# Kernel tuning notes

Measured on AMD Instinct MI355X. Metric: run time of the kernel, lower is better.

## Reference

```python
import jax, jax.numpy as jnp
import numpy as np

B, N, F = 16, 1024, 256
HEADS, K, DOUT = 8, 512, 256
TAU = 1.0
EPS = 1e-08


def setup_inputs() -> dict:
    key = jax.random.key(0)
    k1, k2, k3, k4, k5, k6 = jax.random.split(key, 6)
    return {
        'Q': jax.random.normal(k1, (B, N, F), dtype=jnp.float32),
        'keys': jax.random.uniform(k2, (HEADS, K, F), dtype=jnp.float32),
        'conv_w': jax.random.normal(k3, (HEADS,), dtype=jnp.float32),
        'lin_w': jax.random.normal(k4, (DOUT, F), dtype=jnp.float32) * 0.05,
        'lin_b': jax.random.normal(k5, (DOUT,), dtype=jnp.float32) * 0.05,
        'mask': jax.random.randint(k6, (B, N), 0, 2, dtype=jnp.int32),
    }


def kl_reg(C):
    # C: (B, N, K)
    P = C ** 2
    cn = jnp.sum(C, axis=-2, keepdims=True) + EPS          # sum over N
    P = P / cn
    pn = jnp.sum(P, axis=-1, keepdims=True) + EPS          # sum over K
    P = P / pn
    kl = jnp.sum(P * (jnp.log(P + EPS) - jnp.log(C + EPS)))
    return 100.0 * kl


def memconv_fwd(Q, keys, conv_w, lin_w, lin_b, fmask):
    # pairwise L2 distance Q (B,N,F) vs keys (H,K,F) -> C (B,H,N,K)
    q2 = jnp.sum(Q * Q, axis=-1)                            # (B,N)
    k2 = jnp.sum(keys * keys, axis=-1)                      # (H,K)
    qk = jnp.einsum('bnf,hkf->bhnk', Q, keys)               # (B,H,N,K)
    d2 = q2[:, None, :, None] + k2[None, :, None, :] - 2.0 * qk
    C = jnp.sqrt(jnp.maximum(d2, 0.0))
    em = fmask[:, None, :, None]                            # (B,1,N,1) broadcast
    C = C * em
    # student-t kernel (gmn variant)
    C = (1.0 + C ** 2 / TAU) ** (-(0.5 * TAU + 0.5))
    C = C / jnp.sum(C, axis=-1, keepdims=True)
    C = C * em
    # conv1x1 over heads -> (B,N,K)
    C = jnp.einsum('bhnk,h->bnk', C, conv_w)
    C = jax.nn.softmax(C, axis=-1)
    C = C * fmask[:, :, None]
    kl = kl_reg(C)
    V = jnp.einsum('bnk,bnf->bkf', C, Q)                    # (B,K,F)
    out = jax.nn.leaky_relu(jnp.einsum('bkf,of->bko', V, lin_w) + lin_b, 0.01)
    return out, kl


def reference(Q, keys, conv_w, lin_w, lin_b, mask):
    fmask = mask.astype(Q.dtype)
    return memconv_fwd(Q, keys, conv_w, lin_w, lin_b, fmask)
```

## Files before the change

kernel.cpp:

```cpp
#include <hip/hip_runtime.h>
#include <math.h>

#define Bc 16
#define Nc 1024
#define Fc 256
#define Hc 8
#define Kc 512
#define DOUTc 256
#define EPSc 1e-8f

typedef short v8s __attribute__((ext_vector_type(8)));
typedef float v4f __attribute__((ext_vector_type(4)));

__device__ __forceinline__ float waveReduceSum(float v) {
    v += __shfl_xor(v, 32); v += __shfl_xor(v, 16); v += __shfl_xor(v, 8);
    v += __shfl_xor(v, 4);  v += __shfl_xor(v, 2);  v += __shfl_xor(v, 1);
    return v;
}

__device__ __forceinline__ unsigned short f2bf(float f) {
    unsigned int u = __float_as_uint(f);
    u = (u + 0x7fffu + ((u >> 16) & 1u)) >> 16;
    return (unsigned short)u;
}

__device__ __forceinline__ void lds_barrier() {
    __builtin_amdgcn_s_waitcnt(0xC07F);
    __builtin_amdgcn_s_barrier();
}

__global__ __launch_bounds__(256) void prep_all(
    const float* __restrict__ Q, const float* __restrict__ keys,
    const float* __restrict__ lin_w,
    float* __restrict__ k2g, unsigned short* __restrict__ Kp,
    unsigned short* __restrict__ Qbp, unsigned short* __restrict__ Wp,
    float* __restrict__ cn, float* __restrict__ klout) {
    __shared__ unsigned short T2[32][66];
    const int bx = blockIdx.x;
    const int tid = threadIdx.x;
    if (bx < 1024) {
        int row = bx * 4 + (tid >> 6);
        int l = tid & 63;
        float4 v = *(const float4*)(keys + (size_t)row * Fc + l * 4);
        float s = v.x * v.x + v.y * v.y + v.z * v.z + v.w * v.w;
        s = waveReduceSum(s);
        if (l == 0) k2g[row] = s;
    } else if (bx < 1536) {
        int t = (bx - 1024) * 256 + tid;
        int lane = t & 63, ci = t >> 6;
        int ct = ci & 7, ks = (ci >> 3) & 7, wv = (ci >> 6) & 3, h = ci >> 8;
        int qd = lane >> 4, li = lane & 15;
        int col = h * 512 + wv * 128 + ct * 16 + li;
        const float* src = keys + (size_t)col * Fc + ks * 32 + qd * 8;
        float4 a = *(const float4*)src;
        float4 b = *(const float4*)(src + 4);
        *(ushort4*)(Kp + (size_t)t * 8) = make_ushort4(f2bf(a.x), f2bf(a.y), f2bf(a.z), f2bf(a.w));
        *(ushort4*)(Kp + (size_t)t * 8 + 4) = make_ushort4(f2bf(b.x), f2bf(b.y), f2bf(b.z), f2bf(b.w));
    } else if (bx < 3584) {
        int i = bx - 1536;
        int n0 = (i & 31) * 32, f0 = ((i >> 5) & 3) * 64, bb = i >> 7;
        {
            int n_l = tid >> 3, f_l = (tid & 7) * 8;
            const float* src = Q + ((size_t)(bb * Nc + n0 + n_l)) * Fc + f0 + f_l;
            float4 a = *(const float4*)src;
            float4 b = *(const float4*)(src + 4);
            T2[n_l][f_l + 0] = f2bf(a.x); T2[n_l][f_l + 1] = f2bf(a.y);
            T2[n_l][f_l + 2] = f2bf(a.z); T2[n_l][f_l + 3] = f2bf(a.w);
            T2[n_l][f_l + 4] = f2bf(b.x); T2[n_l][f_l + 5] = f2bf(b.y);
            T2[n_l][f_l + 6] = f2bf(b.z); T2[n_l][f_l + 7] = f2bf(b.w);
        }
        __syncthreads();
        int c = tid >> 6, L = tid & 63;
        int qd = L >> 4, li = L & 15;
        unsigned short o[8];
#pragma unroll
        for (int j = 0; j < 8; j++) o[j] = T2[qd * 8 + j][c * 16 + li];
        size_t idx = ((((size_t)bb * 16 + (f0 >> 4) + c) * 32 + (n0 >> 5)) * 64 + L) * 8;
        *(ushort4*)(Qbp + idx) = make_ushort4(o[0], o[1], o[2], o[3]);
        *(ushort4*)(Qbp + idx + 4) = make_ushort4(o[4], o[5], o[6], o[7]);
    } else if (bx < 3616) {
        int t = (bx - 3584) * 256 + tid;
        int lane = t & 63, ci = t >> 6;
        int ot = ci >> 3, fs = ci & 7;
        int qd = lane >> 4, li = lane & 15;
        const float* src = lin_w + (size_t)(ot * 16 + li) * Fc + fs * 32 + qd * 8;
        float4 a = *(const float4*)src;
        float4 b = *(const float4*)(src + 4);
        *(ushort4*)(Wp + (size_t)t * 8) = make_ushort4(f2bf(a.x), f2bf(a.y), f2bf(a.z), f2bf(a.w));
        *(ushort4*)(Wp + (size_t)t * 8 + 4) = make_ushort4(f2bf(b.x), f2bf(b.y), f2bf(b.z), f2bf(b.w));
    } else {
        int i = (bx - 3616) * 256 + tid;
        float4 z = make_float4(0.f, 0.f, 0.f, 0.f);
        float4* d = (float4*)(cn + (size_t)i * 16);
        d[0] = z; d[1] = z; d[2] = z; d[3] = z;
        if (bx == 3616 && tid == 0) *klout = 0.f;
    }
}

__global__ __launch_bounds__(256, 1) void cmfma_kernel(
    const float* __restrict__ Q, const unsigned short* __restrict__ Kp,
    const float* __restrict__ k2g, const float* __restrict__ conv_w,
    const int* __restrict__ mask, float* __restrict__ C,
    float* __restrict__ cn, unsigned short* __restrict__ Ctp) {
    __shared__ float k2s[Hc * Kc];
    __shared__ float q2s[32];
    __shared__ float msh[32];
    __shared__ float redb[Hc][4][32];
    __shared__ float mslot[4][32];
    __shared__ float eslot[4][32];
    __shared__ short Tb[512][36];
    const int tid = threadIdx.x;
    const int wv = tid >> 6, L = tid & 63;
    const int qd = L >> 4, li = L & 15;
    const int gr0 = blockIdx.x * 32;
    const int b = gr0 >> 10;

    v8s A[2][8];
    {
        float q2part[2] = {0.f, 0.f};
#pragma unroll
        for (int s = 0; s < 2; s++) {
            const float* qrow = Q + (size_t)(gr0 + s * 16 + li) * Fc + qd * 8;
#pragma unroll
            for (int ks = 0; ks < 8; ks++) {
                float4 a = *(const float4*)(qrow + ks * 32);
                float4 bq = *(const float4*)(qrow + ks * 32 + 4);
                v8s f;
                f[0] = (short)f2bf(a.x);  f[1] = (short)f2bf(a.y);
                f[2] = (short)f2bf(a.z);  f[3] = (short)f2bf(a.w);
                f[4] = (short)f2bf(bq.x); f[5] = (short)f2bf(bq.y);
                f[6] = (short)f2bf(bq.z); f[7] = (short)f2bf(bq.w);
                A[s][ks] = f;
                q2part[s] += a.x * a.x + a.y * a.y + a.z * a.z + a.w * a.w +
                             bq.x * bq.x + bq.y * bq.y + bq.z * bq.z + bq.w * bq.w;
            }
            q2part[s] += __shfl_xor(q2part[s], 16);
            q2part[s] += __shfl_xor(q2part[s], 32);
            if (qd == 0 && wv == 0) q2s[s * 16 + li] = q2part[s];
        }
    }
    if (tid < 32) msh[tid] = (float)mask[gr0 + tid];
    for (int i = tid; i < Hc * Kc / 4; i += 256)
        *(float4*)&k2s[i * 4] = *(const float4*)(k2g + i * 4);

    v4f D[2][8], S[2][8];
#pragma unroll
    for (int s = 0; s < 2; s++)
#pragma unroll
        for (int ct = 0; ct < 8; ct++) {
            D[s][ct] = (v4f){0.f, 0.f, 0.f, 0.f};
            S[s][ct] = (v4f){0.f, 0.f, 0.f, 0.f};
        }

    const unsigned short* kwbase = Kp + (size_t)L * 8;
    v8s Bc0[8], Bn[8];
    {
        const unsigned short* p0 = kwbase + (size_t)(wv * 64) * 512;
#pragma unroll
        for (int ct = 0; ct < 8; ct++) Bc0[ct] = *(const v8s*)(p0 + ct * 512);
    }

    lds_barrier();

    float q2r[2][4], mrow[2][4];
#pragma unroll
    for (int s = 0; s < 2; s++)
#pragma unroll
        for (int r = 0; r < 4; r++) {
            q2r[s][r] = q2s[s * 16 + qd * 4 + r];
            mrow[s][r] = msh[s * 16 + qd * 4 + r];
        }

#define KSTEP(kk, CUR, NXT)                                                        \
    do {                                                                           \
        int hn = h * 8 + (kk) + 1;                                                 \
        int hh = (hn >> 3) & 7, kn = hn & 7;                                       \
        const unsigned short* pb =                                                 \
            kwbase + (size_t)(((hh * 4 + wv) * 64 + kn * 8)) * 512;                \
        _Pragma("unroll") for (int ct = 0; ct < 8; ct++)                           \
            NXT[ct] = *(const v8s*)(pb + ct * 512);                                \
        _Pragma("unroll") for (int ct = 0; ct < 8; ct++)                           \
            D[0][ct] = __builtin_amdgcn_mfma_f32_16x16x32_bf16(A[0][kk], CUR[ct],  \
                                                               D[0][ct], 0, 0, 0);\
        _Pragma("unroll") for (int ct = 0; ct < 8; ct++)                           \
            D[1][ct] = __builtin_amdgcn_mfma_f32_16x16x32_bf16(A[1][kk], CUR[ct],  \
                                                               D[1][ct], 0, 0, 0);\
    } while (0)

    for (int h = 0; h < Hc; ++h) {
        KSTEP(0, Bc0, Bn); KSTEP(1, Bn, Bc0);
        KSTEP(2, Bc0, Bn); KSTEP(3, Bn, Bc0);
        KSTEP(4, Bc0, Bn); KSTEP(5, Bn, Bc0);
        KSTEP(6, Bc0, Bn); KSTEP(7, Bn, Bc0);

        float rs[2][4] = {{0.f, 0.f, 0.f, 0.f}, {0.f, 0.f, 0.f, 0.f}};
#pragma unroll
        for (int ct = 0; ct < 8; ct++) {
            float k2v = k2s[h * Kc + wv * 128 + ct * 16 + li];
#pragma unroll
            for (int s = 0; s < 2; s++)
#pragma unroll
                for (int r = 0; r < 4; r++) {
                    float d2 = fmaxf(q2r[s][r] + k2v - 2.f * D[s][ct][r], 0.f) * mrow[s][r];
                    float t = __builtin_amdgcn_rcpf(1.f + d2);
                    D[s][ct][r] = t;
                    rs[s][r] += t;
                }
        }
#pragma unroll
        for (int s = 0; s < 2; s++)
#pragma unroll
            for (int r = 0; r < 4; r++) {
                rs[s][r] += __shfl_xor(rs[s][r], 1, 16);
                rs[s][r] += __shfl_xor(rs[s][r], 2, 16);
                rs[s][r] += __shfl_xor(rs[s][r], 4, 16);
                rs[s][r] += __shfl_xor(rs[s][r], 8, 16);
            }
        if (li == 0) {
#pragma unroll
            for (int s = 0; s < 2; s++)
#pragma unroll
                for (int r = 0; r < 4; r++) redb[h][wv][s * 16 + qd * 4 + r] = rs[s][r];
        }
        lds_barrier();
        float wh = conv_w[h];
        float sc[2][4];
#pragma unroll
        for (int s = 0; s < 2; s++)
#pragma unroll
            for (int r = 0; r < 4; r++) {
                int rw = s * 16 + qd * 4 + r;
                float tot = redb[h][0][rw] + redb[h][1][rw] + redb[h][2][rw] + redb[h][3][rw];
                sc[s][r] = wh * __builtin_amdgcn_rcpf(tot);
            }
#pragma unroll
        for (int s = 0; s < 2; s++)
#pragma unroll
            for (int ct = 0; ct < 8; ct++)
#pragma unroll
                for (int r = 0; r < 4; r++) {
                    S[s][ct][r] += sc[s][r] * D[s][ct][r];
                    D[s][ct][r] = 0.f;
                }
    }
#undef KSTEP

    float mx[2][4] = {{-1e30f, -1e30f, -1e30f, -1e30f}, {-1e30f, -1e30f, -1e30f, -1e30f}};
#pragma unroll
    for (int s = 0; s < 2; s++)
#pragma unroll
        for (int ct = 0; ct < 8; ct++)
#pragma unroll
            for (int r = 0; r < 4; r++) mx[s][r] = fmaxf(mx[s][r], S[s][ct][r]);
#pragma unroll
    for (int s = 0; s < 2; s++)
#pragma unroll
        for (int r = 0; r < 4; r++) {
            mx[s][r] = fmaxf(mx[s][r], __shfl_xor(mx[s][r], 1, 16));
            mx[s][r] = fmaxf(mx[s][r], __shfl_xor(mx[s][r], 2, 16));
            mx[s][r] = fmaxf(mx[s][r], __shfl_xor(mx[s][r], 4, 16));
            mx[s][r] = fmaxf(mx[s][r], __shfl_xor(mx[s][r], 8, 16));
        }
    if (li == 0) {
#pragma unroll
        for (int s = 0; s < 2; s++)
#pragma unroll
            for (int r = 0; r < 4; r++) mslot[wv][s * 16 + qd * 4 + r] = mx[s][r];
    }
    lds_barrier();
#pragma unroll
    for (int s = 0; s < 2; s++)
#pragma unroll
        for (int r = 0; r < 4; r++) {
            int rw = s * 16 + qd * 4 + r;
            mx[s][r] = fmaxf(fmaxf(mslot[0][rw], mslot[1][rw]),
                             fmaxf(mslot[2][rw], mslot[3][rw]));
        }
    float es[2][4] = {{0.f, 0.f, 0.f, 0.f}, {0.f, 0.f, 0.f, 0.f}};
#pragma unroll
    for (int s = 0; s < 2; s++)
#pragma unroll
        for (int ct = 0; ct < 8; ct++)
#pragma unroll
            for (int r = 0; r < 4; r++) {
                float e = __expf(S[s][ct][r] - mx[s][r]);
                S[s][ct][r] = e;
                es[s][r] += e;
            }
#pragma unroll
    for (int s = 0; s < 2; s++)
#pragma unroll
        for (int r = 0; r < 4; r++) {
            es[s][r] += __shfl_xor(es[s][r], 1, 16);
            es[s][r] += __shfl_xor(es[s][r], 2, 16);
            es[s][r] += __shfl_xor(es[s][r], 4, 16);
            es[s][r] += __shfl_xor(es[s][r], 8, 16);
        }
    if (li == 0) {
#pragma unroll
        for (int s = 0; s < 2; s++)
#pragma unroll
            for (int r = 0; r < 4; r++) eslot[wv][s * 16 + qd * 4 + r] = es[s][r];
    }
    lds_barrier();
    float inv[2][4];
#pragma unroll
    for (int s = 0; s < 2; s++)
#pragma unroll
        for (int r = 0; r < 4; r++) {
            int rw = s * 16 + qd * 4 + r;
            float tot = eslot[0][rw] + eslot[1][rw] + eslot[2][rw] + eslot[3][rw];
            inv[s][r] = mrow[s][r] / tot;
        }
#pragma unroll
    for (int ct = 0; ct < 8; ct++) {
        int k = wv * 128 + ct * 16 + li;
        float colsum = 0.f;
#pragma unroll
        for (int s = 0; s < 2; s++) {
            float cv[4];
#pragma unroll
            for (int r = 0; r < 4; r++) {
                cv[r] = S[s][ct][r] * inv[s][r];
                C[(size_t)(gr0 + s * 16 + qd * 4 + r) * Kc + k] = cv[r];
                colsum += cv[r];
            }
            short4 t4;
            t4.x = (short)f2bf(cv[0]); t4.y = (short)f2bf(cv[1]);
            t4.z = (short)f2bf(cv[2]); t4.w = (short)f2bf(cv[3]);
            *(short4*)&Tb[k][s * 16 + qd * 4] = t4;
        }
        colsum += __shfl_xor(colsum, 16);
        colsum += __shfl_xor(colsum, 32);
        if (qd == 0) atomicAdd(&cn[b * Kc + k], colsum);
    }
    lds_barrier();
    {
        const int ns0 = (gr0 & 1023) >> 5;
#pragma unroll
        for (int kk = 0; kk < 2; kk++) {
            int k = tid * 2 + kk;
            int kt = k >> 4, klo = k & 15;
            size_t cbase = (((size_t)b * 32 + kt) * 32 + ns0) * 512;
#pragma unroll
            for (int q2i = 0; q2i < 4; q2i++) {
                short4 lo = *(short4*)&Tb[k][q2i * 8];
                short4 hi = *(short4*)&Tb[k][q2i * 8 + 4];
                short4* d = (short4*)(Ctp + cbase + (size_t)(q2i * 16 + klo) * 8);
                d[0] = lo; d[1] = hi;
            }
        }
    }
}

__global__ __launch_bounds__(256) void klv_kernel(
    const unsigned short* __restrict__ Ctp, const unsigned short* __restrict__ Qbp,
    unsigned short* __restrict__ Vp, const float* __restrict__ C,
    const float* __restrict__ cn, float* __restrict__ klout) {
    __shared__ short Vt[64][76];
    __shared__ float red[4];
    int tid = threadIdx.x;
    int bx = blockIdx.x;
    if (bx < 512) {
        int w = tid >> 6, L = tid & 63;
        int qd = L >> 4, li = L & 15;
        int wr = w >> 1, wc = w & 1;
        int bb = bx >> 5;
        int rem = bx & 31;
        int ktb = rem >> 2, ftb = rem & 3;
        int KT0 = ktb * 4 + wr * 2;
        int FT0 = ftb * 4 + wc * 2;
        const unsigned short* pa0 = Ctp + (((size_t)bb * 32 + KT0) * 32) * 512 + L * 8;
        const unsigned short* pa1 = pa0 + (size_t)32 * 512;
        const unsigned short* pb0 = Qbp + (((size_t)bb * 16 + FT0) * 32) * 512 + L * 8;
        const unsigned short* pb1 = pb0 + (size_t)32 * 512;
        v4f acc[2][2];
#pragma unroll
        for (int a = 0; a < 2; a++)
#pragma unroll
            for (int c = 0; c < 2; c++) acc[a][c] = (v4f){0.f, 0.f, 0.f, 0.f};

        v8s A0 = *(const v8s*)pa0, A1 = *(const v8s*)pa1;
        v8s B0 = *(const v8s*)pb0, B1 = *(const v8s*)pb1;
        for (int ns = 0; ns < 32; ns++) {
            int nsn = (ns + 1) & 31;
            v8s A0n = *(const v8s*)(pa0 + nsn * 512);
            v8s A1n = *(const v8s*)(pa1 + nsn * 512);
            v8s B0n = *(const v8s*)(pb0 + nsn * 512);
            v8s B1n = *(const v8s*)(pb1 + nsn * 512);
            acc[0][0] = __builtin_amdgcn_mfma_f32_16x16x32_bf16(A0, B0, acc[0][0], 0, 0, 0);
            acc[0][1] = __builtin_amdgcn_mfma_f32_16x16x32_bf16(A0, B1, acc[0][1], 0, 0, 0);
            acc[1][0] = __builtin_amdgcn_mfma_f32_16x16x32_bf16(A1, B0, acc[1][0], 0, 0, 0);
            acc[1][1] = __builtin_amdgcn_mfma_f32_16x16x32_bf16(A1, B1, acc[1][1], 0, 0, 0);
            A0 = A0n; A1 = A1n; B0 = B0n; B1 = B1n;
        }
#pragma unroll
        for (int a = 0; a < 2; a++)
#pragma unroll
            for (int c = 0; c < 2; c++)
#pragma unroll
                for (int r = 0; r < 4; r++)
                    Vt[(wr * 2 + a) * 16 + qd * 4 + r][(wc * 2 + c) * 16 + li] =
                        (short)f2bf(acc[a][c][r]);
        __syncthreads();
        {
            int ci = tid >> 5, s5 = tid & 31;
            int mtl = ci >> 1, fsl = ci & 1;
            size_t mt_g = (size_t)bb * 32 + ktb * 4 + mtl;
            size_t fs_g = (size_t)ftb * 2 + fsl;
#pragma unroll
            for (int half = 0; half < 2; half++) {
                int L2 = s5 + half * 32;
                int qd2 = L2 >> 4, li2 = L2 & 15;
                short4 x0 = *(short4*)&Vt[mtl * 16 + li2][fsl * 32 + qd2 * 8];
                short4 x1 = *(short4*)&Vt[mtl * 16 + li2][fsl * 32 + qd2 * 8 + 4];
                short4* d = (short4*)(Vp + ((mt_g * 8 + fs_g) * 64 + L2) * 8);
                d[0] = x0; d[1] = x1;
            }
        }
    } else {
        int bk = bx - 512;
        int w = tid >> 6, l = tid & 63;
        float kacc = 0.f;
#pragma unroll
        for (int rr = 0; rr < 4; rr++) {
            int row = bk * 16 + w * 4 + rr;
            int b = row >> 10;
            const float* cp = C + (size_t)row * Kc + l * 8;
            const float* np = cn + b * Kc + l * 8;
            float4 c0 = *(const float4*)cp;
            float4 c1 = *(const float4*)(cp + 4);
            float4 n0 = *(const float4*)np;
            float4 n1 = *(const float4*)(np + 4);
            float p[8];
            p[0] = c0.x * c0.x / (n0.x + EPSc); p[1] = c0.y * c0.y / (n0.y + EPSc);
            p[2] = c0.z * c0.z / (n0.z + EPSc); p[3] = c0.w * c0.w / (n0.w + EPSc);
            p[4] = c1.x * c1.x / (n1.x + EPSc); p[5] = c1.y * c1.y / (n1.y + EPSc);
            p[6] = c1.z * c1.z / (n1.z + EPSc); p[7] = c1.w * c1.w / (n1.w + EPSc);
            float s = p[0] + p[1] + p[2] + p[3] + p[4] + p[5] + p[6] + p[7];
            float pn = waveReduceSum(s) + EPSc;
            float rpn = 1.0f / pn;
            float cc[8] = {c0.x, c0.y, c0.z, c0.w, c1.x, c1.y, c1.z, c1.w};
#pragma unroll
            for (int j = 0; j < 8; j++) {
                float P = p[j] * rpn;
                kacc += P * __logf((P + EPSc) / (cc[j] + EPSc));
            }
        }
        kacc = waveReduceSum(kacc);
        if (l == 0) red[w] = kacc;
        __syncthreads();
        if (tid == 0)
            atomicAdd(klout, 100.f * (red[0] + red[1] + red[2] + red[3]));
    }
}

__global__ __launch_bounds__(256) void ofma_kernel(
    const unsigned short* __restrict__ Vp, const unsigned short* __restrict__ Wp,
    const float* __restrict__ bias, float* __restrict__ out) {
    int tid = threadIdx.x;
    int w = tid >> 6, L = tid & 63;
    int qd = L >> 4, li = L & 15;
    int wr = w >> 1, wc = w & 1;
    int MT0 = blockIdx.x * 4 + wr * 2;
    int OT0 = blockIdx.y * 4 + wc * 2;
    const unsigned short* pa0 = Vp + ((size_t)MT0 * 8) * 512 + L * 8;
    const unsigned short* pa1 = pa0 + (size_t)8 * 512;
    const unsigned short* pb0 = Wp + ((size_t)OT0 * 8) * 512 + L * 8;
    const unsigned short* pb1 = pb0 + (size_t)8 * 512;
    v4f acc[2][2];
#pragma unroll
    for (int a = 0; a < 2; a++)
#pragma unroll
        for (int c = 0; c < 2; c++) acc[a][c] = (v4f){0.f, 0.f, 0.f, 0.f};
#pragma unroll
    for (int fs = 0; fs < 8; fs++) {
        v8s A0 = *(const v8s*)(pa0 + fs * 512);
        v8s A1 = *(const v8s*)(pa1 + fs * 512);
        v8s B0 = *(const v8s*)(pb0 + fs * 512);
        v8s B1 = *(const v8s*)(pb1 + fs * 512);
        acc[0][0] = __builtin_amdgcn_mfma_f32_16x16x32_bf16(A0, B0, acc[0][0], 0, 0, 0);
        acc[0][1] = __builtin_amdgcn_mfma_f32_16x16x32_bf16(A0, B1, acc[0][1], 0, 0, 0);
        acc[1][0] = __builtin_amdgcn_mfma_f32_16x16x32_bf16(A1, B0, acc[1][0], 0, 0, 0);
        acc[1][1] = __builtin_amdgcn_mfma_f32_16x16x32_bf16(A1, B1, acc[1][1], 0, 0, 0);
    }
#pragma unroll
    for (int c = 0; c < 2; c++) {
        float bv = bias[(OT0 + c) * 16 + li];
#pragma unroll
        for (int a = 0; a < 2; a++)
#pragma unroll
            for (int r = 0; r < 4; r++) {
                int m = (MT0 + a) * 16 + qd * 4 + r;
                int o = (OT0 + c) * 16 + li;
                float x = acc[a][c][r] + bv;
                out[(size_t)m * DOUTc + o] = x > 0.f ? x : 0.01f * x;
            }
    }
}

extern "C" void kernel_launch(void* const* d_in, const int* in_sizes, int n_in,
                              void* d_out, int out_size, void* d_ws, size_t ws_size,
                              hipStream_t stream) {
    const float* Q = (const float*)d_in[0];
    const float* keys = (const float*)d_in[1];
    const float* conv_w = (const float*)d_in[2];
    const float* lin_w = (const float*)d_in[3];
    const float* lin_b = (const float*)d_in[4];
    const int* mask = (const int*)d_in[5];

    float* out = (float*)d_out;
    float* kl = out + (size_t)Bc * Kc * DOUTc;

    float* ws = (float*)d_ws;
    float* C = ws;
    float* k2 = C + (size_t)Bc * Nc * Kc;
    float* cn = k2 + (size_t)Hc * Kc;
    unsigned short* Kp = (unsigned short*)(cn + (size_t)Bc * Kc);
    unsigned short* Ctp = Kp + (size_t)Hc * Kc * Fc;
    unsigned short* Qbp = Ctp + (size_t)Bc * Nc * Kc;
    unsigned short* Vp = Qbp + (size_t)Bc * Nc * Fc;
    unsigned short* Wp = Vp + (size_t)Bc * Kc * Fc;

    prep_all<<<3618, 256, 0, stream>>>(Q, keys, lin_w, k2, Kp, Qbp, Wp, cn, kl);
    cmfma_kernel<<<Bc * Nc / 32, 256, 0, stream>>>(Q, Kp, k2, conv_w, mask, C, cn, Ctp);
    klv_kernel<<<1536, 256, 0, stream>>>(Ctp, Qbp, Vp, C, cn, kl);
    ofma_kernel<<<dim3(Bc * Kc / 64, DOUTc / 64), 256, 0, stream>>>(Vp, Wp, lin_b, out);
}
```

Baseline: 192.6 us.

## Split cmfma row halves across eight waves to raise occupancy

The distance/softmax kernel now runs 512 threads (8 waves) per block instead of 256. Each wave handles one 16-row half of the 32-row tile and a 128-column group, which halves per-thread accumulator and A-fragment registers, and launch bounds allow two blocks per CU. The intent is more waves in flight to hide the global key loads and the reduction barriers. The cost is that each key fragment is now loaded by two waves instead of one, doubling B-operand global traffic per block, and every barrier synchronises more waves.

```diff
diff --git a/kernel.cpp b/kernel.cpp
--- a/kernel.cpp
+++ b/kernel.cpp
@@ -97,7 +97,7 @@
     }
 }
 
-__global__ __launch_bounds__(256, 1) void cmfma_kernel(
+__global__ __launch_bounds__(512, 2) void cmfma_kernel(
     const float* __restrict__ Q, const unsigned short* __restrict__ Kp,
     const float* __restrict__ k2g, const float* __restrict__ conv_w,
     const int* __restrict__ mask, float* __restrict__ C,
@@ -105,86 +105,77 @@
     __shared__ float k2s[Hc * Kc];
     __shared__ float q2s[32];
     __shared__ float msh[32];
-    __shared__ float redb[Hc][4][32];
-    __shared__ float mslot[4][32];
-    __shared__ float eslot[4][32];
+    __shared__ float redb[Hc][4][2][16];
+    __shared__ float mslot[4][2][16];
+    __shared__ float eslot[4][2][16];
     __shared__ short Tb[512][36];
     const int tid = threadIdx.x;
     const int wv = tid >> 6, L = tid & 63;
     const int qd = L >> 4, li = L & 15;
+    const int s = wv & 1, cg = wv >> 1;
     const int gr0 = blockIdx.x * 32;
     const int b = gr0 >> 10;
 
-    v8s A[2][8];
+    v8s A[8];
     {
-        float q2part[2] = {0.f, 0.f};
-#pragma unroll
-        for (int s = 0; s < 2; s++) {
-            const float* qrow = Q + (size_t)(gr0 + s * 16 + li) * Fc + qd * 8;
-#pragma unroll
-            for (int ks = 0; ks < 8; ks++) {
-                float4 a = *(const float4*)(qrow + ks * 32);
-                float4 bq = *(const float4*)(qrow + ks * 32 + 4);
-                v8s f;
-                f[0] = (short)f2bf(a.x);  f[1] = (short)f2bf(a.y);
-                f[2] = (short)f2bf(a.z);  f[3] = (short)f2bf(a.w);
-                f[4] = (short)f2bf(bq.x); f[5] = (short)f2bf(bq.y);
-                f[6] = (short)f2bf(bq.z); f[7] = (short)f2bf(bq.w);
-                A[s][ks] = f;
-                q2part[s] += a.x * a.x + a.y * a.y + a.z * a.z + a.w * a.w +
-                             bq.x * bq.x + bq.y * bq.y + bq.z * bq.z + bq.w * bq.w;
-            }
-            q2part[s] += __shfl_xor(q2part[s], 16);
-            q2part[s] += __shfl_xor(q2part[s], 32);
-            if (qd == 0 && wv == 0) q2s[s * 16 + li] = q2part[s];
-        }
+        float q2part = 0.f;
+        const float* qrow = Q + (size_t)(gr0 + s * 16 + li) * Fc + qd * 8;
+#pragma unroll
+        for (int ks = 0; ks < 8; ks++) {
+            float4 a = *(const float4*)(qrow + ks * 32);
+            float4 bq = *(const float4*)(qrow + ks * 32 + 4);
+            v8s f;
+            f[0] = (short)f2bf(a.x);  f[1] = (short)f2bf(a.y);
+            f[2] = (short)f2bf(a.z);  f[3] = (short)f2bf(a.w);
+            f[4] = (short)f2bf(bq.x); f[5] = (short)f2bf(bq.y);
+            f[6] = (short)f2bf(bq.z); f[7] = (short)f2bf(bq.w);
+            A[ks] = f;
+            q2part += a.x * a.x + a.y * a.y + a.z * a.z + a.w * a.w +
+                      bq.x * bq.x + bq.y * bq.y + bq.z * bq.z + bq.w * bq.w;
+        }
+        q2part += __shfl_xor(q2part, 16);
+        q2part += __shfl_xor(q2part, 32);
+        if (cg == 0 && qd == 0) q2s[s * 16 + li] = q2part;
     }
     if (tid < 32) msh[tid] = (float)mask[gr0 + tid];
-    for (int i = tid; i < Hc * Kc / 4; i += 256)
+    for (int i = tid; i < Hc * Kc / 4; i += 512)
         *(float4*)&k2s[i * 4] = *(const float4*)(k2g + i * 4);
 
-    v4f D[2][8], S[2][8];
-#pragma unroll
-    for (int s = 0; s < 2; s++)
-#pragma unroll
-        for (int ct = 0; ct < 8; ct++) {
-            D[s][ct] = (v4f){0.f, 0.f, 0.f, 0.f};
-            S[s][ct] = (v4f){0.f, 0.f, 0.f, 0.f};
-        }
+    v4f D[8], S[8];
+#pragma unroll
+    for (int ct = 0; ct < 8; ct++) {
+        D[ct] = (v4f){0.f, 0.f, 0.f, 0.f};
+        S[ct] = (v4f){0.f, 0.f, 0.f, 0.f};
+    }
 
     const unsigned short* kwbase = Kp + (size_t)L * 8;
     v8s Bc0[8], Bn[8];
     {
-        const unsigned short* p0 = kwbase + (size_t)(wv * 64) * 512;
+        const unsigned short* p0 = kwbase + (size_t)(cg * 64) * 512;
 #pragma unroll
         for (int ct = 0; ct < 8; ct++) Bc0[ct] = *(const v8s*)(p0 + ct * 512);
     }
 
     lds_barrier();
 
-    float q2r[2][4], mrow[2][4];
-#pragma unroll
-    for (int s = 0; s < 2; s++)
-#pragma unroll
-        for (int r = 0; r < 4; r++) {
-            q2r[s][r] = q2s[s * 16 + qd * 4 + r];
-            mrow[s][r] = msh[s * 16 + qd * 4 + r];
-        }
+    float q2r[4], mrow[4];
+#pragma unroll
+    for (int r = 0; r < 4; r++) {
+        q2r[r] = q2s[s * 16 + qd * 4 + r];
+        mrow[r] = msh[s * 16 + qd * 4 + r];
+    }
 
 #define KSTEP(kk, CUR, NXT)                                                        \
     do {                                                                           \
         int hn = h * 8 + (kk) + 1;                                                 \
         int hh = (hn >> 3) & 7, kn = hn & 7;                                       \
         const unsigned short* pb =                                                 \
-            kwbase + (size_t)(((hh * 4 + wv) * 64 + kn * 8)) * 512;                \
+            kwbase + (size_t)(((hh * 4 + cg) * 64 + kn * 8)) * 512;                \
         _Pragma("unroll") for (int ct = 0; ct < 8; ct++)                           \
             NXT[ct] = *(const v8s*)(pb + ct * 512);                                \
         _Pragma("unroll") for (int ct = 0; ct < 8; ct++)                           \
-            D[0][ct] = __builtin_amdgcn_mfma_f32_16x16x32_bf16(A[0][kk], CUR[ct],  \
-                                                               D[0][ct], 0, 0, 0);\
-        _Pragma("unroll") for (int ct = 0; ct < 8; ct++)                           \
-            D[1][ct] = __builtin_amdgcn_mfma_f32_16x16x32_bf16(A[1][kk], CUR[ct],  \
-                                                               D[1][ct], 0, 0, 0);\
+            D[ct] = __builtin_amdgcn_mfma_f32_16x16x32_bf16(A[kk], CUR[ct],        \
+                                                            D[ct], 0, 0, 0);      \
     } while (0)
 
     for (int h = 0; h < Hc; ++h) {
@@ -193,162 +184,132 @@
         KSTEP(4, Bc0, Bn); KSTEP(5, Bn, Bc0);
         KSTEP(6, Bc0, Bn); KSTEP(7, Bn, Bc0);
 
-        float rs[2][4] = {{0.f, 0.f, 0.f, 0.f}, {0.f, 0.f, 0.f, 0.f}};
+        float rs[4] = {0.f, 0.f, 0.f, 0.f};
 #pragma unroll
         for (int ct = 0; ct < 8; ct++) {
-            float k2v = k2s[h * Kc + wv * 128 + ct * 16 + li];
-#pragma unroll
-            for (int s = 0; s < 2; s++)
-#pragma unroll
-                for (int r = 0; r < 4; r++) {
-                    float d2 = fmaxf(q2r[s][r] + k2v - 2.f * D[s][ct][r], 0.f) * mrow[s][r];
-                    float t = __builtin_amdgcn_rcpf(1.f + d2);
-                    D[s][ct][r] = t;
-                    rs[s][r] += t;
-                }
-        }
-#pragma unroll
-        for (int s = 0; s < 2; s++)
+            float k2v = k2s[h * Kc + cg * 128 + ct * 16 + li];
 #pragma unroll
             for (int r = 0; r < 4; r++) {
-                rs[s][r] += __shfl_xor(rs[s][r], 1, 16);
-                rs[s][r] += __shfl_xor(rs[s][r], 2, 16);
-                rs[s][r] += __shfl_xor(rs[s][r], 4, 16);
-                rs[s][r] += __shfl_xor(rs[s][r], 8, 16);
+                float d2 = fmaxf(q2r[r] + k2v - 2.f * D[ct][r], 0.f) * mrow[r];
+                float t = __builtin_amdgcn_rcpf(1.f + d2);
+                D[ct][r] = t;
+                rs[r] += t;
             }
+        }
+#pragma unroll
+        for (int r = 0; r < 4; r++) {
+            rs[r] += __shfl_xor(rs[r], 1, 16);
+            rs[r] += __shfl_xor(rs[r], 2, 16);
+            rs[r] += __shfl_xor(rs[r], 4, 16);
+            rs[r] += __shfl_xor(rs[r], 8, 16);
+        }
         if (li == 0) {
 #pragma unroll
-            for (int s = 0; s < 2; s++)
-#pragma unroll
-                for (int r = 0; r < 4; r++) redb[h][wv][s * 16 + qd * 4 + r] = rs[s][r];
+            for (int r = 0; r < 4; r++) redb[h][cg][s][qd * 4 + r] = rs[r];
         }
         lds_barrier();
         float wh = conv_w[h];
-        float sc[2][4];
-#pragma unroll
-        for (int s = 0; s < 2; s++)
+        float sc[4];
+#pragma unroll
+        for (int r = 0; r < 4; r++) {
+            int rw = qd * 4 + r;
+            float tot = redb[h][0][s][rw] + redb[h][1][s][rw] +
+                        redb[h][2][s][rw] + redb[h][3][s][rw];
+            sc[r] = wh * __builtin_amdgcn_rcpf(tot);
+        }
+#pragma unroll
+        for (int ct = 0; ct < 8; ct++)
 #pragma unroll
             for (int r = 0; r < 4; r++) {
-                int rw = s * 16 + qd * 4 + r;
-                float tot = redb[h][0][rw] + redb[h][1][rw] + redb[h][2][rw] + redb[h][3][rw];
-                sc[s][r] = wh * __builtin_amdgcn_rcpf(tot);
+                S[ct][r] += sc[r] * D[ct][r];
+                D[ct][r] = 0.f;
             }
-#pragma unroll
-        for (int s = 0; s < 2; s++)
-#pragma unroll
-            for (int ct = 0; ct < 8; ct++)
-#pragma unroll
-                for (int r = 0; r < 4; r++) {
-                    S[s][ct][r] += sc[s][r] * D[s][ct][r];
-                    D[s][ct][r] = 0.f;
-                }
     }
 #undef KSTEP
 
-    float mx[2][4] = {{-1e30f, -1e30f, -1e30f, -1e30f}, {-1e30f, -1e30f, -1e30f, -1e30f}};
-#pragma unroll
-    for (int s = 0; s < 2; s++)
-#pragma unroll
-        for (int ct = 0; ct < 8; ct++)
-#pragma unroll
-            for (int r = 0; r < 4; r++) mx[s][r] = fmaxf(mx[s][r], S[s][ct][r]);
-#pragma unroll
-    for (int s = 0; s < 2; s++)
+    float mx[4] = {-1e30f, -1e30f, -1e30f, -1e30f};
+#pragma unroll
+    for (int ct = 0; ct < 8; ct++)
+#pragma unroll
+        for (int r = 0; r < 4; r++) mx[r] = fmaxf(mx[r], S[ct][r]);
+#pragma unroll
+    for (int r = 0; r < 4; r++) {
+        mx[r] = fmaxf(mx[r], __shfl_xor(mx[r], 1, 16));
+        mx[r] = fmaxf(mx[r], __shfl_xor(mx[r], 2, 16));
+        mx[r] = fmaxf(mx[r], __shfl_xor(mx[r], 4, 16));
+        mx[r] = fmaxf(mx[r], __shfl_xor(mx[r], 8, 16));
+    }
+    if (li == 0) {
+#pragma unroll
+        for (int r = 0; r < 4; r++) mslot[cg][s][qd * 4 + r] = mx[r];
+    }
+    lds_barrier();
+#pragma unroll
+    for (int r = 0; r < 4; r++) {
+        int rw = qd * 4 + r;
+        mx[r] = fmaxf(fmaxf(mslot[0][s][rw], mslot[1][s][rw]),
+                      fmaxf(mslot[2][s][rw], mslot[3][s][rw]));
+    }
+    float es[4] = {0.f, 0.f, 0.f, 0.f};
+#pragma unroll
+    for (int ct = 0; ct < 8; ct++)
 #pragma unroll
         for (int r = 0; r < 4; r++) {
-            mx[s][r] = fmaxf(mx[s][r], __shfl_xor(mx[s][r], 1, 16));
-            mx[s][r] = fmaxf(mx[s][r], __shfl_xor(mx[s][r], 2, 16));
-            mx[s][r] = fmaxf(mx[s][r], __shfl_xor(mx[s][r], 4, 16));
-            mx[s][r] = fmaxf(mx[s][r], __shfl_xor(mx[s][r], 8, 16));
-        }
+            float e = __expf(S[ct][r] - mx[r]);
+            S[ct][r] = e;
+            es[r] += e;
+        }
+#pragma unroll
+    for (int r = 0; r < 4; r++) {
+        es[r] += __shfl_xor(es[r], 1, 16);
+        es[r] += __shfl_xor(es[r], 2, 16);
+        es[r] += __shfl_xor(es[r], 4, 16);
+        es[r] += __shfl_xor(es[r], 8, 16);
+    }
     if (li == 0) {
 #pragma unroll
-        for (int s = 0; s < 2; s++)
-#pragma unroll
-            for (int r = 0; r < 4; r++) mslot[wv][s * 16 + qd * 4 + r] = mx[s][r];
+        for (int r = 0; r < 4; r++) eslot[cg][s][qd * 4 + r] = es[r];
     }
     lds_barrier();
-#pragma unroll
-    for (int s = 0; s < 2; s++)
+    float inv[4];
+#pragma unroll
+    for (int r = 0; r < 4; r++) {
+        int rw = qd * 4 + r;
+        float tot = eslot[0][s][rw] + eslot[1][s][rw] +
+                    eslot[2][s][rw] + eslot[3][s][rw];
+        inv[r] = mrow[r] / tot;
+    }
+#pragma unroll
+    for (int ct = 0; ct < 8; ct++) {
+        int k = cg * 128 + ct * 16 + li;
+        float cv[4];
+        float colsum = 0.f;
 #pragma unroll
         for (int r = 0; r < 4; r++) {
-            int rw = s * 16 + qd * 4 + r;
-            mx[s][r] = fmaxf(fmaxf(mslot[0][rw], mslot[1][rw]),
-                             fmaxf(mslot[2][rw], mslot[3][rw]));
-        }
-    float es[2][4] = {{0.f, 0.f, 0.f, 0.f}, {0.f, 0.f, 0.f, 0.f}};
-#pragma unroll
-    for (int s = 0; s < 2; s++)
-#pragma unroll
-        for (int ct = 0; ct < 8; ct++)
-#pragma unroll
-            for (int r = 0; r < 4; r++) {
-                float e = __expf(S[s][ct][r] - mx[s][r]);
-                S[s][ct][r] = e;
-                es[s][r] += e;
-            }
-#pragma unroll
-    for (int s = 0; s < 2; s++)
-#pragma unroll
-        for (int r = 0; r < 4; r++) {
-            es[s][r] += __shfl_xor(es[s][r], 1, 16);
-            es[s][r] += __shfl_xor(es[s][r], 2, 16);
-            es[s][r] += __shfl_xor(es[s][r], 4, 16);
-            es[s][r] += __shfl_xor(es[s][r], 8, 16);
-        }
-    if (li == 0) {
-#pragma unroll
-        for (int s = 0; s < 2; s++)
-#pragma unroll
-            for (int r = 0; r < 4; r++) eslot[wv][s * 16 + qd * 4 + r] = es[s][r];
-    }
-    lds_barrier();
-    float inv[2][4];
-#pragma unroll
-    for (int s = 0; s < 2; s++)
-#pragma unroll
-        for (int r = 0; r < 4; r++) {
-            int rw = s * 16 + qd * 4 + r;
-            float tot = eslot[0][rw] + eslot[1][rw] + eslot[2][rw] + eslot[3][rw];
-            inv[s][r] = mrow[s][r] / tot;
-        }
-#pragma unroll
-    for (int ct = 0; ct < 8; ct++) {
-        int k = wv * 128 + ct * 16 + li;
-        float colsum = 0.f;
-#pragma unroll
-        for (int s = 0; s < 2; s++) {
-            float cv[4];
-#pragma unroll
-            for (int r = 0; r < 4; r++) {
-                cv[r] = S[s][ct][r] * inv[s][r];
-                C[(size_t)(gr0 + s * 16 + qd * 4 + r) * Kc + k] = cv[r];
-                colsum += cv[r];
-            }
-            short4 t4;
-            t4.x = (short)f2bf(cv[0]); t4.y = (short)f2bf(cv[1]);
-            t4.z = (short)f2bf(cv[2]); t4.w = (short)f2bf(cv[3]);
-            *(short4*)&Tb[k][s * 16 + qd * 4] = t4;
-        }
+            cv[r] = S[ct][r] * inv[r];
+            C[(size_t)(gr0 + s * 16 + qd * 4 + r) * Kc + k] = cv[r];
+            colsum += cv[r];
+        }
+        short4 t4;
+        t4.x = (short)f2bf(cv[0]); t4.y = (short)f2bf(cv[1]);
+        t4.z = (short)f2bf(cv[2]); t4.w = (short)f2bf(cv[3]);
+        *(short4*)&Tb[k][s * 16 + qd * 4] = t4;
         colsum += __shfl_xor(colsum, 16);
         colsum += __shfl_xor(colsum, 32);
         if (qd == 0) atomicAdd(&cn[b * Kc + k], colsum);
     }
     lds_barrier();
-    {
+    if (tid < 512) {
         const int ns0 = (gr0 & 1023) >> 5;
-#pragma unroll
-        for (int kk = 0; kk < 2; kk++) {
-            int k = tid * 2 + kk;
-            int kt = k >> 4, klo = k & 15;
-            size_t cbase = (((size_t)b * 32 + kt) * 32 + ns0) * 512;
-#pragma unroll
-            for (int q2i = 0; q2i < 4; q2i++) {
-                short4 lo = *(short4*)&Tb[k][q2i * 8];
-                short4 hi = *(short4*)&Tb[k][q2i * 8 + 4];
-                short4* d = (short4*)(Ctp + cbase + (size_t)(q2i * 16 + klo) * 8);
-                d[0] = lo; d[1] = hi;
-            }
+        int k = tid;
+        int kt = k >> 4, klo = k & 15;
+        size_t cbase = (((size_t)b * 32 + kt) * 32 + ns0) * 512;
+#pragma unroll
+        for (int q2i = 0; q2i < 4; q2i++) {
+            short4 lo = *(short4*)&Tb[k][q2i * 8];
+            short4 hi = *(short4*)&Tb[k][q2i * 8 + 4];
+            short4* d = (short4*)(Ctp + cbase + (size_t)(q2i * 16 + klo) * 8);
+            d[0] = lo; d[1] = hi;
         }
     }
 }
@@ -523,7 +484,7 @@
     unsigned short* Wp = Vp + (size_t)Bc * Kc * Fc;
 
     prep_all<<<3618, 256, 0, stream>>>(Q, keys, lin_w, k2, Kp, Qbp, Wp, cn, kl);
-    cmfma_kernel<<<Bc * Nc / 32, 256, 0, stream>>>(Q, Kp, k2, conv_w, mask, C, cn, Ctp);
+    cmfma_kernel<<<Bc * Nc / 32, 512, 0, stream>>>(Q, Kp, k2, conv_w, mask, C, cn, Ctp);
     klv_kernel<<<1536, 256, 0, stream>>>(Ctp, Qbp, Vp, C, cn, kl);
     ofma_kernel<<<dim3(Bc * Kc / 64, DOUTc / 64), 256, 0, stream>>>(Vp, Wp, lin_b, out);
 }
```

Result: slower. 200.0 us (+3.9%).
